# Optimization experiments

Measured on AMD Instinct MI355X. Metric: run time of the kernel, lower is better.

Reference implementation:

```python
import jax, jax.numpy as jnp
import numpy as np
from jax import lax

B, C, H, W = 4, 512, 48, 48
R = 8            # inter_rate -> spatial q/k channels = C // R
C4 = C // 4      # chl_attention query channels
N = H * W


def _conv1x1(x, w, b=None):
    # x: (B,C,H,W), w: (O,C)
    y = jnp.einsum('bchw,oc->bohw', x, w)
    if b is not None:
        y = y + b[None, :, None, None]
    return y


def _conv3x3(x, w):
    # w: (O,I,3,3), SAME padding, no bias
    return lax.conv_general_dilated(x, w, (1, 1), 'SAME',
                                    dimension_numbers=('NCHW', 'OIHW', 'NCHW'))


def _bn_relu(x, scale, bias):
    # eval-mode BatchNorm folded into per-channel scale/bias, then ReLU
    return jax.nn.relu(x * scale[None, :, None, None] + bias[None, :, None, None])


def _masked_softmax(e, mask):
    # softmax restricted to mask>0 positions (== exp(e)*mask / sum(exp(e)*mask))
    neg = jnp.finfo(e.dtype).min
    z = jnp.where(mask[None] > 0, e, neg)
    return jax.nn.softmax(z, axis=-1)


def _chl(x, qw, qs, qb, ew, eb):
    # channel attention block (chl_attention)
    b, c, h, w = x.shape
    n = h * w
    q = jnp.einsum('bchw,oc->bohw', x, qw)                 # (B,C4,H,W)
    q = jax.nn.relu(q * qs[None, :, None, None] + qb[None, :, None, None])
    q = q.reshape(b, C4, n)
    k = x.reshape(b, c, n)
    energy = jnp.einsum('bqn,bcn->bqc', q, k)              # (B,C4,C)
    expand = jnp.einsum('oq,bqc->boc', ew, energy) + eb[None, :, None]  # (B,C,C)
    en = jnp.max(expand, -1, keepdims=True) - expand
    attn = jax.nn.softmax(en, -1)                          # (B,C,C)
    out = jnp.einsum('bcd,bdn->bcn', attn, k)
    return out.reshape(b, c, h, w)


def setup_inputs() -> dict:
    key = jax.random.key(0)
    ks = jax.random.split(key, 32)
    f = jnp.float32
    s = lambda k, shp, sc: (sc * jax.random.normal(k, shp)).astype(f)
    inp = {}
    inp['x'] = s(ks[0], (B, C, H, W), 1.0)
    Cr = C // R
    inp['wq'] = s(ks[1], (Cr, C), 1.0 / np.sqrt(C))
    inp['bq'] = s(ks[2], (Cr,), 0.02)
    inp['wk'] = s(ks[3], (Cr, C), 1.0 / np.sqrt(C))
    inp['bk'] = s(ks[4], (Cr,), 0.02)
    inp['wv0'] = s(ks[5], (C, C), 1.0 / np.sqrt(C))
    inp['bv0'] = s(ks[6], (C,), 0.02)
    inp['conv1_w'] = s(ks[7], (C, C, 3, 3), 1.0 / np.sqrt(9 * C))
    inp['conv1_s'] = (1.0 + 0.1 * jax.random.normal(ks[8], (C,))).astype(f)
    inp['conv1_b'] = s(ks[9], (C,), 0.05)
    inp['conv2_w'] = s(ks[10], (C, C, 3, 3), 1.0 / np.sqrt(9 * C))
    inp['conv2_s'] = (1.0 + 0.1 * jax.random.normal(ks[11], (C,))).astype(f)
    inp['conv2_b'] = s(ks[12], (C,), 0.05)
    inp['gamma'] = jnp.full((1,), 0.5, f)
    inp['gamma1'] = jnp.full((1,), 0.5, f)
    inp['gamma2'] = jnp.full((1,), 0.5, f)
    # chl_attention #1 params
    inp['c1_qw'] = s(ks[13], (C4, C), 1.0 / np.sqrt(C))
    inp['c1_qs'] = (1.0 + 0.1 * jax.random.normal(ks[14], (C4,))).astype(f)
    inp['c1_qb'] = s(ks[15], (C4,), 0.05)
    inp['c1_ew'] = s(ks[16], (C, C4), 1.0 / np.sqrt(C4))
    inp['c1_eb'] = s(ks[17], (C,), 0.02)
    # chl_attention #2 params
    inp['c2_qw'] = s(ks[18], (C4, C), 1.0 / np.sqrt(C))
    inp['c2_qs'] = (1.0 + 0.1 * jax.random.normal(ks[19], (C4,))).astype(f)
    inp['c2_qb'] = s(ks[20], (C4,), 0.05)
    inp['c2_ew'] = s(ks[21], (C, C4), 1.0 / np.sqrt(C4))
    inp['c2_eb'] = s(ks[22], (C,), 0.02)
    # binary (N,N) masks: random sparsity + diagonal so every row has support
    eye = jnp.eye(N, dtype=f)
    m1 = (jax.random.uniform(ks[23], (N, N)) < 0.25).astype(f)
    m2 = (jax.random.uniform(ks[24], (N, N)) < 0.10).astype(f)
    inp['mask1'] = jnp.maximum(m1, eye)
    inp['mask2'] = jnp.maximum(m2, eye)
    return inp


def reference(x, wq, bq, wk, bk, wv0, bv0, conv1_w, conv1_s, conv1_b,
              conv2_w, conv2_s, conv2_b, gamma, gamma1, gamma2,
              c1_qw, c1_qs, c1_qb, c1_ew, c1_eb,
              c2_qw, c2_qs, c2_qb, c2_ew, c2_eb, mask1, mask2):
    b, c, h, w = x.shape
    n = h * w
    q = _conv1x1(x, wq, bq).reshape(b, -1, n)   # (B,Cr,N)
    k = _conv1x1(x, wk, bk).reshape(b, -1, n)   # (B,Cr,N)
    energy = jnp.einsum('bqn,bqm->bnm', q, k)   # (B,N,N)
    attn0 = jax.nn.softmax(energy, -1)
    attn1 = _masked_softmax(energy, mask1)
    attn2 = _masked_softmax(energy, mask2)
    v = _conv1x1(x, wv0, bv0).reshape(b, c, n)
    # pass 0 (unmasked)
    out0 = jnp.einsum('bcn,bmn->bcm', v, attn0).reshape(b, c, h, w)
    out0 = gamma[0] * out0 + x
    out0 = _bn_relu(_conv3x3(out0, conv1_w), conv1_s, conv1_b)
    # pass 1 (mask1, channel-attn value)
    v1 = _chl(out0, c1_qw, c1_qs, c1_qb, c1_ew, c1_eb).reshape(b, c, n)
    out1 = jnp.einsum('bcn,bmn->bcm', v1, attn1).reshape(b, c, h, w)
    out1 = gamma1[0] * out1 + out0
    out1 = _bn_relu(_conv3x3(out1, conv2_w), conv2_s, conv2_b)
    # pass 2 (mask2)
    v2 = _chl(out1, c2_qw, c2_qs, c2_qb, c2_ew, c2_eb).reshape(b, c, n)
    out2 = jnp.einsum('bcn,bmn->bcm', v2, attn2).reshape(b, c, h, w)
    out = gamma2[0] * out2 + out1
    return out
```

## Files before the change

kernel.cpp:

```cpp
#include <hip/hip_runtime.h>

#define B_  4
#define C_  512
#define H_  48
#define W_  48
#define N_  2304
#define CR_ 64
#define C4_ 128
#define TK  16
#define LDSP 68
#define PW  50
#define PN  2500
#define KW  4608

typedef short  s16x8 __attribute__((ext_vector_type(8)));
typedef float  f32x4 __attribute__((ext_vector_type(4)));

__device__ __forceinline__ unsigned short f2bf(float f) {
  union { float f; unsigned int u; } v; v.f = f;
  const unsigned int u = v.u;
  return (unsigned short)((u + 0x7FFFu + ((u >> 16) & 1u)) >> 16);
}
__device__ __forceinline__ float bf2f(unsigned short h) {
  union { unsigned int u; float f; } v; v.u = ((unsigned int)h) << 16;
// ... 356 lines not shown
      acc[1][0] = __builtin_amdgcn_mfma_f32_16x16x32_bf16(ah1, bl0, acc[1][0], 0, 0, 0);
      acc[1][1] = __builtin_amdgcn_mfma_f32_16x16x32_bf16(ah1, bl1, acc[1][1], 0, 0, 0);
      acc[0][0] = __builtin_amdgcn_mfma_f32_16x16x32_bf16(al0, bh0, acc[0][0], 0, 0, 0);
      acc[0][1] = __builtin_amdgcn_mfma_f32_16x16x32_bf16(al0, bh1, acc[0][1], 0, 0, 0);
      acc[1][0] = __builtin_amdgcn_mfma_f32_16x16x32_bf16(al1, bh0, acc[1][0], 0, 0, 0);
      acc[1][1] = __builtin_amdgcn_mfma_f32_16x16x32_bf16(al1, bh1, acc[1][1], 0, 0, 0);
    }
    __syncthreads();
  }

  float* Yb = Y + (size_t)b * ySB;
#pragma unroll
  for (int mt = 0; mt < 2; ++mt)
#pragma unroll
    for (int nt = 0; nt < 2; ++nt) {
      const int col = n0 + wn * 32 + nt * 16 + lrow;
      const int rbase = m0 + wm * 32 + mt * 16 + (lane >> 4) * 4;
#pragma unroll
      for (int i = 0; i < 4; ++i) {
        const int row = rbase + i;
        float v = acc[mt][nt][i];
        const float s  = scale ? scale[row] : 1.f;
        const float bb = bias ? bias[row] : 0.f;
        v = v * s + bb;
        if (relu) v = fmaxf(v, 0.f);
        if (outMode == 0)      Yb[(size_t)row * ldy + col] = v;
        else if (outMode == 1) Yb[(size_t)col * ldy + row] = v;
        else                   atomicAdd(Yb + (size_t)col * ldy + row, v);
      }
    }
}

__global__ __launch_bounds__(256)
void pad_split(const float* __restrict__ X, unsigned short* __restrict__ Xh,
               unsigned short* __restrict__ Xl)
{
  __shared__ float t[64][65];
  const int b = blockIdx.x, n0 = blockIdx.y * 64;
  const int tid = threadIdx.x;
  const float* Xb = X + (size_t)b * C_ * N_;
  unsigned short* Xhb = Xh + (size_t)b * PN * C_;
  unsigned short* Xlb = Xl + (size_t)b * PN * C_;
  for (int cs = 0; cs < 8; ++cs) {
    const int c0 = cs * 64;
    __syncthreads();
#pragma unroll
    for (int i = 0; i < 16; ++i) {
      const int cc = i * 4 + (tid >> 6);
      t[cc][tid & 63] = Xb[(size_t)(c0 + cc) * N_ + n0 + (tid & 63)];
    }
    __syncthreads();
    const int cc = tid & 63;
#pragma unroll
    for (int i = 0; i < 16; ++i) {
      const int nn = i * 4 + (tid >> 6);
      const int n = n0 + nn;
      const float v = t[cc][nn];
      const unsigned short hh = f2bf(v);
      const unsigned short ll = f2bf(v - bf2f(hh));
      const size_t p = (size_t)((n / 48 + 1) * PW + (n % 48) + 1) * C_ + c0 + cc;
      Xhb[p] = hh; Xlb[p] = ll;
    }
  }
}

__global__ __launch_bounds__(256)
void zero_ring(unsigned short* __restrict__ Xh, unsigned short* __restrict__ Xl)
{
  const int b = blockIdx.y, r = blockIdx.x;
  int pcol;
  if (r < 50)       pcol = r;
  else if (r < 100) pcol = 49 * PW + (r - 50);
  else if (r < 148) pcol = (r - 100 + 1) * PW;
  else              pcol = (r - 148 + 1) * PW + 49;
  unsigned int* h = (unsigned int*)(Xh + ((size_t)b * PN + pcol) * C_);
  unsigned int* l = (unsigned int*)(Xl + ((size_t)b * PN + pcol) * C_);
  h[threadIdx.x] = 0u;
  l[threadIdx.x] = 0u;
}

__global__ __launch_bounds__(256)
void wsplit(const float* __restrict__ W, unsigned short* __restrict__ Wh,
            unsigned short* __restrict__ Wl)
{
  const int o = blockIdx.x, tap = blockIdx.y;
#pragma unroll
  for (int i = 0; i < 2; ++i) {
    const int c = threadIdx.x + i * 256;
    const float v = W[(size_t)o * KW + c * 9 + tap];
    const unsigned short hh = f2bf(v);
    Wh[(size_t)o * KW + tap * C_ + c] = hh;
    Wl[(size_t)o * KW + tap * C_ + c] = f2bf(v - bf2f(hh));
  }
}

__global__ __launch_bounds__(256)
void tr_split(const float* __restrict__ X, unsigned short* __restrict__ Th,
              unsigned short* __restrict__ Tl)
{
  __shared__ float t[64][65];
  const int b = blockIdx.x, n0 = blockIdx.y * 64;
  const int tid = threadIdx.x;
  const float* Xb = X + (size_t)b * C_ * N_;
  unsigned short* Thb = Th + (size_t)b * N_ * C_;
  unsigned short* Tlb = Tl + (size_t)b * N_ * C_;
  for (int cs = 0; cs < 8; ++cs) {
    const int c0 = cs * 64;
    __syncthreads();
#pragma unroll
    for (int i = 0; i < 16; ++i) {
      const int cc = i * 4 + (tid >> 6);
      t[cc][tid & 63] = Xb[(size_t)(c0 + cc) * N_ + n0 + (tid & 63)];
    }
    __syncthreads();
    const int cc = tid & 63;
#pragma unroll
    for (int i = 0; i < 16; ++i) {
      const int nn = i * 4 + (tid >> 6);
      const float v = t[cc][nn];
      const unsigned short hh = f2bf(v);
      Thb[(size_t)(n0 + nn) * C_ + c0 + cc] = hh;
      Tlb[(size_t)(n0 + nn) * C_ + c0 + cc] = f2bf(v - bf2f(hh));
    }
  }
}

__global__ __launch_bounds__(256)
void mfma_conv2(const unsigned short* __restrict__ Xh, const unsigned short* __restrict__ Xl,
                const unsigned short* __restrict__ Wh, const unsigned short* __restrict__ Wl,
                const float* __restrict__ sc, const float* __restrict__ bi,
                float* __restrict__ Y)
{
  __shared__ unsigned short Ah[64][72], Al[64][72];
  __shared__ unsigned short Bh[64][72], Bl[64][72];
  const int b  = blockIdx.z;
  const int m0 = blockIdx.y * 64, n0 = blockIdx.x * 64;
  const int tid  = threadIdx.x;
  const int lane = tid & 63, wave = tid >> 6;
  const int wm = wave >> 1, wn = wave & 1;
  const int lrow = lane & 15, lk8 = (lane >> 4) * 8;
  const int sRow = tid >> 2, sK = (tid & 3) * 16;
  const int nj = n0 + sRow;
  const int pbase = (nj / 48 + 1) * PW + (nj % 48) + 1;
  const unsigned short* Xhb = Xh + (size_t)b * PN * C_;
  const unsigned short* Xlb = Xl + (size_t)b * PN * C_;
  f32x4 acc[2][2] = {};
  s16x8 r0, r1, r2, r3, r4, r5, r6, r7;

#define CONV_LD(IT)                                                        \
  {                                                                        \
    const int tap_ = (IT) >> 3, c0_ = ((IT) & 7) * 64;                     \
    const int t3_ = tap_ / 3;                                              \
    const int toff_ = (t3_ - 1) * PW + (tap_ - t3_ * 3 - 1);               \
    const size_t bofs_ = (size_t)(pbase + toff_) * C_ + c0_ + sK;          \
    const size_t wrow_ = (size_t)(m0 + sRow) * KW + (size_t)tap_ * C_ + c0_ + sK; \
    r0 = *(const s16x8*)(Wh + wrow_);     r1 = *(const s16x8*)(Wh + wrow_ + 8); \
    r2 = *(const s16x8*)(Wl + wrow_);     r3 = *(const s16x8*)(Wl + wrow_ + 8); \
    r4 = *(const s16x8*)(Xhb + bofs_);    r5 = *(const s16x8*)(Xhb + bofs_ + 8); \
    r6 = *(const s16x8*)(Xlb + bofs_);    r7 = *(const s16x8*)(Xlb + bofs_ + 8); \
  }

  CONV_LD(0);
  for (int it = 0; it < 72; ++it) {
    *(s16x8*)&Ah[sRow][sK] = r0; *(s16x8*)&Ah[sRow][sK + 8] = r1;
    *(s16x8*)&Al[sRow][sK] = r2; *(s16x8*)&Al[sRow][sK + 8] = r3;
    *(s16x8*)&Bh[sRow][sK] = r4; *(s16x8*)&Bh[sRow][sK + 8] = r5;
    *(s16x8*)&Bl[sRow][sK] = r6; *(s16x8*)&Bl[sRow][sK + 8] = r7;
    __syncthreads();
    if (it < 71) CONV_LD(it + 1);
#pragma unroll
    for (int kc = 0; kc < 2; ++kc) {
      const s16x8 ah0 = *(const s16x8*)&Ah[wm * 32 + lrow     ][kc * 32 + lk8];
      const s16x8 ah1 = *(const s16x8*)&Ah[wm * 32 + 16 + lrow][kc * 32 + lk8];
      const s16x8 al0 = *(const s16x8*)&Al[wm * 32 + lrow     ][kc * 32 + lk8];
      const s16x8 al1 = *(const s16x8*)&Al[wm * 32 + 16 + lrow][kc * 32 + lk8];
      const s16x8 bh0 = *(const s16x8*)&Bh[wn * 32 + lrow     ][kc * 32 + lk8];
      const s16x8 bh1 = *(const s16x8*)&Bh[wn * 32 + 16 + lrow][kc * 32 + lk8];
      const s16x8 bl0 = *(const s16x8*)&Bl[wn * 32 + lrow     ][kc * 32 + lk8];
      const s16x8 bl1 = *(const s16x8*)&Bl[wn * 32 + 16 + lrow][kc * 32 + lk8];
      acc[0][0] = __builtin_amdgcn_mfma_f32_16x16x32_bf16(ah0, bh0, acc[0][0], 0, 0, 0);
      acc[0][1] = __builtin_amdgcn_mfma_f32_16x16x32_bf16(ah0, bh1, acc[0][1], 0, 0, 0);
      acc[1][0] = __builtin_amdgcn_mfma_f32_16x16x32_bf16(ah1, bh0, acc[1][0], 0, 0, 0);
      acc[1][1] = __builtin_amdgcn_mfma_f32_16x16x32_bf16(ah1, bh1, acc[1][1], 0, 0, 0);
      acc[0][0] = __builtin_amdgcn_mfma_f32_16x16x32_bf16(ah0, bl0, acc[0][0], 0, 0, 0);
      acc[0][1] = __builtin_amdgcn_mfma_f32_16x16x32_bf16(ah0, bl1, acc[0][1], 0, 0, 0);
      acc[1][0] = __builtin_amdgcn_mfma_f32_16x16x32_bf16(ah1, bl0, acc[1][0], 0, 0, 0);
      acc[1][1] = __builtin_amdgcn_mfma_f32_16x16x32_bf16(ah1, bl1, acc[1][1], 0, 0, 0);
      acc[0][0] = __builtin_amdgcn_mfma_f32_16x16x32_bf16(al0, bh0, acc[0][0], 0, 0, 0);
      acc[0][1] = __builtin_amdgcn_mfma_f32_16x16x32_bf16(al0, bh1, acc[0][1], 0, 0, 0);
      acc[1][0] = __builtin_amdgcn_mfma_f32_16x16x32_bf16(al1, bh0, acc[1][0], 0, 0, 0);
      acc[1][1] = __builtin_amdgcn_mfma_f32_16x16x32_bf16(al1, bh1, acc[1][1], 0, 0, 0);
    }
    __syncthreads();
  }
#undef CONV_LD

  float* Yb = Y + (size_t)b * C_ * N_;
#pragma unroll
  for (int mt = 0; mt < 2; ++mt)
#pragma unroll
    for (int nt = 0; nt < 2; ++nt) {
      const int col = n0 + wn * 32 + nt * 16 + lrow;
      const int rbase = m0 + wm * 32 + mt * 16 + (lane >> 4) * 4;
#pragma unroll
      for (int i = 0; i < 4; ++i) {
        const int row = rbase + i;
        const float v = fmaxf(acc[mt][nt][i] * sc[row] + bi[row], 0.f);
        Yb[(size_t)row * N_ + col] = v;
      }
    }
}

__global__ __launch_bounds__(256)
void mfma_conv_split(const float* __restrict__ X, const float* __restrict__ Wt,
                     const float* __restrict__ sc, const float* __restrict__ bi,
                     float* __restrict__ Y)
{
  __shared__ unsigned short Ah[64][72], Al[64][72];
  __shared__ unsigned short Bh[64][72], Bl[64][72];
  const int b  = blockIdx.z;
  const int m0 = blockIdx.y * 64, n0 = blockIdx.x * 64;
  const int tid  = threadIdx.x;
  const int lane = tid & 63, wave = tid >> 6;
  const int wm = wave >> 1, wn = wave & 1;
  const int lrow = lane & 15, lk8 = (lane >> 4) * 8;
  const int sRow = tid >> 2, sK = (tid & 3) * 16;
  const int tj = tid & 63, tkg = (tid >> 6) * 16;
  const int n = n0 + tj, yy = n / W_, xx = n - yy * W_;
  const float* Xb = X + (size_t)b * C_ * N_;
  f32x4 acc[2][2] = {};

  for (int k0 = 0; k0 < KW; k0 += 64) {
    {
      const float* src = Wt + (size_t)(m0 + sRow) * KW + k0 + sK;
      unsigned short h[16], l[16];
#pragma unroll
      for (int t = 0; t < 16; ++t) {
        const float v = src[t];
        const unsigned short hh = f2bf(v);
        h[t] = hh;
        l[t] = f2bf(v - bf2f(hh));
      }
      *(s16x8*)&Ah[sRow][sK]     = *(s16x8*)&h[0];
      *(s16x8*)&Ah[sRow][sK + 8] = *(s16x8*)&h[8];
      *(s16x8*)&Al[sRow][sK]     = *(s16x8*)&l[0];
      *(s16x8*)&Al[sRow][sK + 8] = *(s16x8*)&l[8];
    }
    {
#pragma unroll
      for (int ii = 0; ii < 16; ii += 2) {
        unsigned int ph = 0, pl = 0;
#pragma unroll
        for (int hft = 0; hft < 2; ++hft) {
          const int kg = k0 + tkg + ii + hft;
          const int c = kg / 9, tap = kg - c * 9;
          const int t3 = tap / 3;
          const int iy = yy + t3 - 1, ix = xx + (tap - t3 * 3) - 1;
          float v = 0.f;
          if (iy >= 0 && iy < H_ && ix >= 0 && ix < W_)
            v = Xb[(size_t)c * N_ + iy * W_ + ix];
          const unsigned short hh = f2bf(v);
          const unsigned short ll = f2bf(v - bf2f(hh));
          ph |= ((unsigned int)hh) << (16 * hft);
          pl |= ((unsigned int)ll) << (16 * hft);
        }
        *(unsigned int*)&Bh[tj][tkg + ii] = ph;
        *(unsigned int*)&Bl[tj][tkg + ii] = pl;
      }
    }
    __syncthreads();
#pragma unroll
    for (int kc = 0; kc < 2; ++kc) {
      const s16x8 ah0 = *(const s16x8*)&Ah[wm * 32 + lrow     ][kc * 32 + lk8];
      const s16x8 ah1 = *(const s16x8*)&Ah[wm * 32 + 16 + lrow][kc * 32 + lk8];
      const s16x8 al0 = *(const s16x8*)&Al[wm * 32 + lrow     ][kc * 32 + lk8];
      const s16x8 al1 = *(const s16x8*)&Al[wm * 32 + 16 + lrow][kc * 32 + lk8];
      const s16x8 bh0 = *(const s16x8*)&Bh[wn * 32 + lrow     ][kc * 32 + lk8];
      const s16x8 bh1 = *(const s16x8*)&Bh[wn * 32 + 16 + lrow][kc * 32 + lk8];
      const s16x8 bl0 = *(const s16x8*)&Bl[wn * 32 + lrow     ][kc * 32 + lk8];
      const s16x8 bl1 = *(const s16x8*)&Bl[wn * 32 + 16 + lrow][kc * 32 + lk8];
      acc[0][0] = __builtin_amdgcn_mfma_f32_16x16x32_bf16(ah0, bh0, acc[0][0], 0, 0, 0);
      acc[0][1] = __builtin_amdgcn_mfma_f32_16x16x32_bf16(ah0, bh1, acc[0][1], 0, 0, 0);
      acc[1][0] = __builtin_amdgcn_mfma_f32_16x16x32_bf16(ah1, bh0, acc[1][0], 0, 0, 0);
      acc[1][1] = __builtin_amdgcn_mfma_f32_16x16x32_bf16(ah1, bh1, acc[1][1], 0, 0, 0);
      acc[0][0] = __builtin_amdgcn_mfma_f32_16x16x32_bf16(ah0, bl0, acc[0][0], 0, 0, 0);
      acc[0][1] = __builtin_amdgcn_mfma_f32_16x16x32_bf16(ah0, bl1, acc[0][1], 0, 0, 0);
      acc[1][0] = __builtin_amdgcn_mfma_f32_16x16x32_bf16(ah1, bl0, acc[1][0], 0, 0, 0);
      acc[1][1] = __builtin_amdgcn_mfma_f32_16x16x32_bf16(ah1, bl1, acc[1][1], 0, 0, 0);
      acc[0][0] = __builtin_amdgcn_mfma_f32_16x16x32_bf16(al0, bh0, acc[0][0], 0, 0, 0);
      acc[0][1] = __builtin_amdgcn_mfma_f32_16x16x32_bf16(al0, bh1, acc[0][1], 0, 0, 0);
      acc[1][0] = __builtin_amdgcn_mfma_f32_16x16x32_bf16(al1, bh0, acc[1][0], 0, 0, 0);
      acc[1][1] = __builtin_amdgcn_mfma_f32_16x16x32_bf16(al1, bh1, acc[1][1], 0, 0, 0);
    }
    __syncthreads();
  }

  float* Yb = Y + (size_t)b * C_ * N_;
#pragma unroll
  for (int mt = 0; mt < 2; ++mt)
#pragma unroll
    for (int nt = 0; nt < 2; ++nt) {
      const int col = n0 + wn * 32 + nt * 16 + lrow;
      const int rbase = m0 + wm * 32 + mt * 16 + (lane >> 4) * 4;
#pragma unroll
      for (int i = 0; i < 4; ++i) {
        const int row = rbase + i;
        const float v = fmaxf(acc[mt][nt][i] * sc[row] + bi[row], 0.f);
        Yb[(size_t)row * N_ + col] = v;
      }
    }
}

__global__ __launch_bounds__(256)
void build_P(const float* __restrict__ E, const float* __restrict__ st,
             int variant, const float* __restrict__ mask,
             unsigned short* __restrict__ P)
{
  const int m = blockIdx.x, b = blockIdx.y, t = threadIdx.x;
  const float* sp = st + ((size_t)b * N_ + m) * 6 + variant * 2;
  const float mx = sp[0], rs = 1.f / sp[1];
  const float* Er = E + ((size_t)b * N_ + m) * N_;
  unsigned short* Pr = P + ((size_t)b * N_ + m) * N_;
  const float* Mr = mask ? mask + (size_t)m * N_ : nullptr;
#pragma unroll
  for (int i = 0; i < 9; ++i) {
    const int idx = t + i * 256;
    float w = __expf(Er[idx] - mx) * rs;
    if (Mr && !(Mr[idx] > 0.f)) w = 0.f;
    Pr[idx] = f2bf(w);
  }
}

__global__ __launch_bounds__(256)
void softmax_stats(const float* __restrict__ E, const float* __restrict__ M1,
                   const float* __restrict__ M2, float* __restrict__ st)
{
  const int row = blockIdx.x, b = blockIdx.y, tid = threadIdx.x;
  const float* er = E + ((size_t)b * N_ + row) * N_;
  const float* r1 = M1 + (size_t)row * N_;
  const float* r2 = M2 + (size_t)row * N_;
  float mx0 = -3.4e38f, mx1 = -3.4e38f, mx2 = -3.4e38f;
  for (int n = tid; n < N_; n += 256) {
    const float v = er[n];
    mx0 = fmaxf(mx0, v);
    if (r1[n] > 0.f) mx1 = fmaxf(mx1, v);
    if (r2[n] > 0.f) mx2 = fmaxf(mx2, v);
  }
  __shared__ float red[256];
  mx0 = blockReduceMax(mx0, red);
  mx1 = blockReduceMax(mx1, red);
  mx2 = blockReduceMax(mx2, red);
  float s0 = 0.f, s1 = 0.f, s2 = 0.f;
  for (int n = tid; n < N_; n += 256) {
    const float v = er[n];
    s0 += __expf(v - mx0);
    if (r1[n] > 0.f) s1 += __expf(v - mx1);
    if (r2[n] > 0.f) s2 += __expf(v - mx2);
  }
  s0 = blockReduceSum(s0, red);
  s1 = blockReduceSum(s1, red);
  s2 = blockReduceSum(s2, red);
  if (tid == 0) {
    float* o = st + ((size_t)b * N_ + row) * 6;
// ... 226 lines not shown
  const float* c2w    = (const float*)d_in[10];
  const float* c2s    = (const float*)d_in[11];
  const float* c2b    = (const float*)d_in[12];
  const float* gamma  = (const float*)d_in[13];
  const float* gamma1 = (const float*)d_in[14];
  const float* gamma2 = (const float*)d_in[15];
  const float* c1qw   = (const float*)d_in[16];
  const float* c1qs   = (const float*)d_in[17];
  const float* c1qb   = (const float*)d_in[18];
  const float* c1ew   = (const float*)d_in[19];
  const float* c1eb   = (const float*)d_in[20];
  const float* c2qw   = (const float*)d_in[21];
  const float* c2qs   = (const float*)d_in[22];
  const float* c2qb   = (const float*)d_in[23];
  const float* c2ew   = (const float*)d_in[24];
  const float* c2eb   = (const float*)d_in[25];
  const float* mask1  = (const float*)d_in[26];
  const float* mask2  = (const float*)d_in[27];

  const size_t QK = 589824;
  const size_t CQ = 1179648;
  const size_t VV = 4718592;
  const size_t EE = 21233664;
  const size_t ST = 55296;
  const size_t CE = 262144;
  const size_t CA = 1048576;
  const size_t ELEMS_B = CQ + VV + EE + ST + VV + CE + CA;
  const size_t ELEMS_A = ELEMS_B + EE / 2;
  const int tier = (ws_size >= ELEMS_A * 4) ? 0
                 : (ws_size >= ELEMS_B * 4) ? 1 : 2;

  float* ws = (float*)d_ws;
  float *qbuf, *kbuf, *cq, *vbuf, *ebuf, *stb, *o0, *ce1, *cat_;
  unsigned short *Pbuf = nullptr, *Xh = nullptr, *Xl = nullptr,
                 *Whs = nullptr, *Wls = nullptr,
                 *xTh = nullptr, *xTl = nullptr, *oTh = nullptr, *oTl = nullptr;
  float *qTf = nullptr, *kTf = nullptr;
  if (tier <= 1) {
    qbuf = ws; kbuf = ws + QK;
    cq   = ws;
    vbuf = ws + CQ;
    ebuf = vbuf + VV;
    stb  = ebuf + EE;
    o0   = stb + ST;
    ce1  = o0 + VV;
    cat_ = ce1 + CE;
    if (tier == 0) {
      unsigned short* reg = (unsigned short*)(cat_ + CA);
      xTh = reg;
      xTl = reg + 4718592;
      qTf = (float*)(reg + 9437184);
      kTf = qTf + 589824;
      Pbuf = reg;
      Xh  = reg;
      Xl  = reg + 5120000;
      Whs = reg + 10240000;
      Wls = reg + 12599296;
      oTh = reg;
      oTl = reg + 4718592;
    }
  } else {
    qbuf = ws; kbuf = qbuf + QK;
    cq   = kbuf + QK;
    vbuf = cq + CQ;
    stb  = vbuf + VV;
    o0   = stb + ST;
    ce1  = o0 + VV;
    cat_ = ce1 + CE;
    ebuf = nullptr;
  }
  float* t0 = (float*)d_out;
  unsigned short* vb16 = (unsigned short*)vbuf;

  const dim3 TPB(256);
  const long long sxc = (long long)C_ * N_;
  const long long sqr = (long long)CR_ * N_;
  const long long sq4 = (long long)C4_ * N_;
  const long long sNN = (long long)N_ * N_;
  const long long sNC = (long long)N_ * C_;
  const long long sCC = (long long)C_ * C_;
  const long long sEC = (long long)C4_ * C_;
  const long long sNR = (long long)N_ * CR_;

  if (tier == 0) {
    tr_split<<<dim3(B_, 36), TPB, 0, stream>>>(x, xTh, xTl);
    mfma_sp<<<dim3(36, 1, 4), TPB, 0, stream>>>(wq, 0, C_, xTh, xTl, sNC, C_, 1,
        qTf, sNR, CR_, 1, C_, 1, nullptr, bq, 0);
    mfma_sp<<<dim3(36, 1, 4), TPB, 0, stream>>>(wk, 0, C_, xTh, xTl, sNC, C_, 1,
        kTf, sNR, CR_, 1, C_, 1, nullptr, bk, 0);
    mfma_gemm<<<dim3(36, 8, 4), TPB, 0, stream>>>(wv0, 0, 0, C_, xTh, sNC, C_, 2,
        vb16, 1, sxc, N_, C_, nullptr, bv0, 0, nullptr, nullptr, 0);
    mfma_sp<<<dim3(36, 36, 4), TPB, 0, stream>>>(qTf, sNR, CR_, kTf, nullptr, sNR, CR_, 0,
        ebuf, sNN, N_, 0, CR_, 1, nullptr, nullptr, 0);
    softmax_stats<<<dim3(N_, 4), TPB, 0, stream>>>(ebuf, mask1, mask2, stb);
  } else if (tier == 1) {
    gemm_nn<<<dim3(36, 1, 4), TPB, 0, stream>>>(wq, 0, C_, x, sxc, N_,
                                                qbuf, sqr, N_, C_, nullptr, bq, 0);
    gemm_nn<<<dim3(36, 1, 4), TPB, 0, stream>>>(wk, 0, C_, x, sxc, N_,
                                                kbuf, sqr, N_, C_, nullptr, bk, 0);
    mfma_gemm<<<dim3(36, 8, 4), TPB, 0, stream>>>(wv0, 0, 0, C_, x, sxc, N_, 1,
        vbuf, 0, sxc, N_, C_, nullptr, bv0, 0, nullptr, nullptr, 0);
    gemm_tn<<<dim3(36, 36, 4), TPB, 0, stream>>>(qbuf, sqr, N_, kbuf, sqr, N_,
                                                 ebuf, sNN, N_, CR_);
    softmax_stats<<<dim3(N_, 4), TPB, 0, stream>>>(ebuf, mask1, mask2, stb);
  } else {
    gemm_nn<<<dim3(36, 1, 4), TPB, 0, stream>>>(wq, 0, C_, x, sxc, N_,
                                                qbuf, sqr, N_, C_, nullptr, bq, 0);
    gemm_nn<<<dim3(36, 1, 4), TPB, 0, stream>>>(wk, 0, C_, x, sxc, N_,
                                                kbuf, sqr, N_, C_, nullptr, bk, 0);
    mfma_gemm<<<dim3(36, 8, 4), TPB, 0, stream>>>(wv0, 0, 0, C_, x, sxc, N_, 1,
        vbuf, 0, sxc, N_, C_, nullptr, bv0, 0, nullptr, nullptr, 0);
    softmax_stats_rq<<<dim3(N_, 4), TPB, 0, stream>>>(qbuf, kbuf, mask1, mask2, stb);
  }

  for (int pass = 0; pass < 3; ++pass) {
    const float* msk = (pass == 0) ? nullptr : (pass == 1 ? mask1 : mask2);
    const float* gm  = (pass == 0) ? gamma : (pass == 1 ? gamma1 : gamma2);
    const float* res = (pass == 0) ? x : o0;
    float* dst = (pass == 2) ? (float*)d_out : t0;

    if (tier == 0) {
      build_P<<<dim3(N_, 4), TPB, 0, stream>>>(ebuf, stb, pass, msk, Pbuf);
      mfma_gemm<<<dim3(36, 8, 4), TPB, 0, stream>>>(vb16, 1, sxc, N_, Pbuf, sNN, N_, 2,
          dst, 0, sxc, N_, N_, nullptr, nullptr, 0, gm, res, sxc);
    } else if (tier == 1) {
      attn_apply<<<dim3(36, 8, 4), TPB, 0, stream>>>(vbuf, ebuf, stb, pass, msk,
                                                     gm, res, dst);
    } else {
      attn_apply_rq<<<dim3(36, 8, 4), TPB, 0, stream>>>(vbuf, qbuf, kbuf, stb, pass, msk,
                                                        gm, res, dst);
    }
    if (pass == 2) break;

    const float* cw = (pass == 0) ? c1w : c2w;
    const float* cs = (pass == 0) ? c1s : c2s;
    const float* cb = (pass == 0) ? c1b : c2b;
    if (tier == 0) {
      pad_split<<<dim3(B_, 36), TPB, 0, stream>>>(dst, Xh, Xl);
      zero_ring<<<dim3(196, B_), TPB, 0, stream>>>(Xh, Xl);
      wsplit<<<dim3(512, 9), TPB, 0, stream>>>(cw, Whs, Wls);
      mfma_conv2<<<dim3(36, 8, 4), TPB, 0, stream>>>(Xh, Xl, Whs, Wls, cs, cb, o0);
    } else {
      mfma_conv_split<<<dim3(36, 8, 4), TPB, 0, stream>>>(dst, cw, cs, cb, o0);
    }

    const float* qw = (pass == 0) ? c1qw : c2qw;
    const float* qs = (pass == 0) ? c1qs : c2qs;
    const float* qb = (pass == 0) ? c1qb : c2qb;
    const float* ew = (pass == 0) ? c1ew : c2ew;
    const float* eb = (pass == 0) ? c1eb : c2eb;
    if (tier == 0) {
      tr_split<<<dim3(B_, 36), TPB, 0, stream>>>(o0, oTh, oTl);
      mfma_sp<<<dim3(36, 2, 4), TPB, 0, stream>>>(qw, 0, C_, oTh, oTl, sNC, C_, 1,
          cq, sq4, N_, 0, C_, 1, qs, qb, 1);
      zero_buf<<<dim3(256), TPB, 0, stream>>>((float4*)ce1, (int)(CE / 4));
      mfma_sp<<<dim3(8, 2, 16), TPB, 0, stream>>>(cq, sq4, N_, o0, nullptr, sxc, N_, 0,
          ce1, sEC, C4_, 2, N_, 4, nullptr, nullptr, 0);
      mfma_sp<<<dim3(8, 8, 4), TPB, 0, stream>>>(ew, 0, C4_, ce1, nullptr, sEC, C4_, 0,
          cat_, sCC, C_, 0, C4_, 1, nullptr, eb, 0);
      chl_softmax<<<dim3(C_ * 4), TPB, 0, stream>>>(cat_);
      mfma_gemm<<<dim3(36, 8, 4), TPB, 0, stream>>>(cat_, 0, sCC, C_, oTh, sNC, C_, 2,
          vb16, 1, sxc, N_, C_, nullptr, nullptr, 0, nullptr, nullptr, 0);
    } else {
      gemm_nn<<<dim3(36, 2, 4), TPB, 0, stream>>>(qw, 0, C_, o0, sxc, N_,
                                                  cq, sq4, N_, C_, qs, qb, 1);
      zero_buf<<<dim3(256), TPB, 0, stream>>>((float4*)ce1, (int)(CE / 4));
      gemm_nt_splitk<<<dim3(8, 2, 16), TPB, 0, stream>>>(cq, sq4, N_, o0, sxc, N_,
                                                         ce1, sEC, C_, N_);
      gemm_nn<<<dim3(8, 8, 4), TPB, 0, stream>>>(ew, 0, C4_, ce1, sEC, C_,
                                                 cat_, sCC, C_, C4_, nullptr, eb, 0);
      chl_softmax<<<dim3(C_ * 4), TPB, 0, stream>>>(cat_);
      mfma_gemm<<<dim3(36, 8, 4), TPB, 0, stream>>>(cat_, 0, sCC, C_, o0, sxc, N_, 1,
          vbuf, 0, sxc, N_, C_, nullptr, nullptr, 0, nullptr, nullptr, 0);
    }
  }
// ... 2 lines not shown
```

Baseline: 1.305 ms.

## Fuse softmax weights into attention-apply GEMM, widen conv tiles, hoist weight splits

```diff
diff --git a/kernel.cpp b/kernel.cpp
--- a/kernel.cpp
+++ b/kernel.cpp
@@ -412,15 +412,29 @@
 }
 
 __global__ __launch_bounds__(256)
-void pad_split(const float* __restrict__ X, unsigned short* __restrict__ Xh,
-               unsigned short* __restrict__ Xl)
-{
-  __shared__ float t[64][65];
-  const int b = blockIdx.x, n0 = blockIdx.y * 64;
+void pad_split2(const float* __restrict__ X, unsigned short* __restrict__ Xh,
+                unsigned short* __restrict__ Xl)
+{
+  const int b = blockIdx.x;
   const int tid = threadIdx.x;
-  const float* Xb = X + (size_t)b * C_ * N_;
   unsigned short* Xhb = Xh + (size_t)b * PN * C_;
   unsigned short* Xlb = Xl + (size_t)b * PN * C_;
+  if (blockIdx.y == 36) {
+    for (int idx = tid; idx < 196 * 256; idx += 256) {
+      const int r = idx >> 8, u = idx & 255;
+      int pcol;
+      if (r < 50)       pcol = r;
+      else if (r < 100) pcol = 49 * PW + (r - 50);
+      else if (r < 148) pcol = (r - 100 + 1) * PW;
+      else              pcol = (r - 148 + 1) * PW + 49;
+      ((unsigned int*)(Xhb + (size_t)pcol * C_))[u] = 0u;
+      ((unsigned int*)(Xlb + (size_t)pcol * C_))[u] = 0u;
+    }
+    return;
+  }
+  __shared__ float t[64][65];
+  const int n0 = blockIdx.y * 64;
+  const float* Xb = X + (size_t)b * C_ * N_;
   for (int cs = 0; cs < 8; ++cs) {
     const int c0 = cs * 64;
     __syncthreads();
@@ -445,21 +459,6 @@
 }
 
 __global__ __launch_bounds__(256)
-void zero_ring(unsigned short* __restrict__ Xh, unsigned short* __restrict__ Xl)
-{
-  const int b = blockIdx.y, r = blockIdx.x;
-  int pcol;
-  if (r < 50)       pcol = r;
-  else if (r < 100) pcol = 49 * PW + (r - 50);
-  else if (r < 148) pcol = (r - 100 + 1) * PW;
-  else              pcol = (r - 148 + 1) * PW + 49;
-  unsigned int* h = (unsigned int*)(Xh + ((size_t)b * PN + pcol) * C_);
-  unsigned int* l = (unsigned int*)(Xl + ((size_t)b * PN + pcol) * C_);
-  h[threadIdx.x] = 0u;
-  l[threadIdx.x] = 0u;
-}
-
-__global__ __launch_bounds__(256)
 void wsplit(const float* __restrict__ W, unsigned short* __restrict__ Wh,
             unsigned short* __restrict__ Wl)
 {
@@ -506,10 +505,209 @@
 }
 
 __global__ __launch_bounds__(256)
-void mfma_conv2(const unsigned short* __restrict__ Xh, const unsigned short* __restrict__ Xl,
+void mfma_conv3(const unsigned short* __restrict__ Xh, const unsigned short* __restrict__ Xl,
                 const unsigned short* __restrict__ Wh, const unsigned short* __restrict__ Wl,
                 const float* __restrict__ sc, const float* __restrict__ bi,
                 float* __restrict__ Y)
+{
+  __shared__ unsigned short Ah[128][72], Al[128][72];
+  __shared__ unsigned short Bh[64][72], Bl[64][72];
+  const int b  = blockIdx.z;
+  const int m0 = blockIdx.y * 128, n0 = blockIdx.x * 64;
+  const int tid  = threadIdx.x;
+  const int lane = tid & 63, wave = tid >> 6;
+  const int wm = wave >> 1, wn = wave & 1;
+  const int lrow = lane & 15, lk8 = (lane >> 4) * 8;
+  const int aRow = tid >> 1, aK = (tid & 1) * 32;
+  const int bRow = tid >> 2, bK = (tid & 3) * 16;
+  const int nj = n0 + bRow;
+  const int pbase = (nj / 48 + 1) * PW + (nj % 48) + 1;
+  const unsigned short* Xhb = Xh + (size_t)b * PN * C_;
+  const unsigned short* Xlb = Xl + (size_t)b * PN * C_;
+  f32x4 acc[4][2] = {};
+  s16x8 a0h, a1h, a2h, a3h, a0l, a1l, a2l, a3l, b0h, b1h, b0l, b1l;
+
+#define CONV_LD(IT)                                                             \
+  {                                                                             \
+    const int tap_ = (IT) >> 3, c0_ = ((IT) & 7) * 64;                          \
+    const int t3_ = tap_ / 3;                                                   \
+    const int toff_ = (t3_ - 1) * PW + (tap_ - t3_ * 3 - 1);                    \
+    const size_t bofs_ = (size_t)(pbase + toff_) * C_ + c0_ + bK;               \
+    const size_t wrow_ = (size_t)(m0 + aRow) * KW + (size_t)tap_ * C_ + c0_ + aK; \
+    a0h = *(const s16x8*)(Wh + wrow_);      a1h = *(const s16x8*)(Wh + wrow_ + 8);  \
+    a2h = *(const s16x8*)(Wh + wrow_ + 16); a3h = *(const s16x8*)(Wh + wrow_ + 24); \
+    a0l = *(const s16x8*)(Wl + wrow_);      a1l = *(const s16x8*)(Wl + wrow_ + 8);  \
+    a2l = *(const s16x8*)(Wl + wrow_ + 16); a3l = *(const s16x8*)(Wl + wrow_ + 24); \
+    b0h = *(const s16x8*)(Xhb + bofs_);     b1h = *(const s16x8*)(Xhb + bofs_ + 8); \
+    b0l = *(const s16x8*)(Xlb + bofs_);     b1l = *(const s16x8*)(Xlb + bofs_ + 8); \
+  }
+
+  CONV_LD(0);
+  for (int it = 0; it < 72; ++it) {
+    *(s16x8*)&Ah[aRow][aK]      = a0h; *(s16x8*)&Ah[aRow][aK + 8]  = a1h;
+    *(s16x8*)&Ah[aRow][aK + 16] = a2h; *(s16x8*)&Ah[aRow][aK + 24] = a3h;
+    *(s16x8*)&Al[aRow][aK]      = a0l; *(s16x8*)&Al[aRow][aK + 8]  = a1l;
+    *(s16x8*)&Al[aRow][aK + 16] = a2l; *(s16x8*)&Al[aRow][aK + 24] = a3l;
+    *(s16x8*)&Bh[bRow][bK]      = b0h; *(s16x8*)&Bh[bRow][bK + 8]  = b1h;
+    *(s16x8*)&Bl[bRow][bK]      = b0l; *(s16x8*)&Bl[bRow][bK + 8]  = b1l;
+    __syncthreads();
+    if (it < 71) CONV_LD(it + 1);
+#pragma unroll
+    for (int kc = 0; kc < 2; ++kc) {
+      s16x8 ah[4], al[4], bh[2], bl[2];
+#pragma unroll
+      for (int mt = 0; mt < 4; ++mt) {
+        ah[mt] = *(const s16x8*)&Ah[wm * 64 + mt * 16 + lrow][kc * 32 + lk8];
+        al[mt] = *(const s16x8*)&Al[wm * 64 + mt * 16 + lrow][kc * 32 + lk8];
+      }
+#pragma unroll
+      for (int nt = 0; nt < 2; ++nt) {
+        bh[nt] = *(const s16x8*)&Bh[wn * 32 + nt * 16 + lrow][kc * 32 + lk8];
+        bl[nt] = *(const s16x8*)&Bl[wn * 32 + nt * 16 + lrow][kc * 32 + lk8];
+      }
+#pragma unroll
+      for (int mt = 0; mt < 4; ++mt)
+#pragma unroll
+        for (int nt = 0; nt < 2; ++nt) {
+          acc[mt][nt] = __builtin_amdgcn_mfma_f32_16x16x32_bf16(ah[mt], bh[nt], acc[mt][nt], 0, 0, 0);
+          acc[mt][nt] = __builtin_amdgcn_mfma_f32_16x16x32_bf16(ah[mt], bl[nt], acc[mt][nt], 0, 0, 0);
+          acc[mt][nt] = __builtin_amdgcn_mfma_f32_16x16x32_bf16(al[mt], bh[nt], acc[mt][nt], 0, 0, 0);
+        }
+    }
+    __syncthreads();
+  }
+#undef CONV_LD
+
+  float* Yb = Y + (size_t)b * C_ * N_;
+#pragma unroll
+  for (int mt = 0; mt < 4; ++mt)
+#pragma unroll
+    for (int nt = 0; nt < 2; ++nt) {
+      const int col = n0 + wn * 32 + nt * 16 + lrow;
+      const int rbase = m0 + wm * 64 + mt * 16 + (lane >> 4) * 4;
+#pragma unroll
+      for (int i = 0; i < 4; ++i) {
+        const int row = rbase + i;
+        const float v = fmaxf(acc[mt][nt][i] * sc[row] + bi[row], 0.f);
+        Yb[(size_t)row * N_ + col] = v;
+      }
+    }
+}
+
+__global__ __launch_bounds__(256)
+void mfma_apply(const unsigned short* __restrict__ V, const float* __restrict__ E,
+                const float* __restrict__ st, int variant,
+                const float* __restrict__ mask,
+                const float* __restrict__ gammaPtr,
+                const float* __restrict__ Resid, float* __restrict__ Y)
+{
+  __shared__ unsigned short As[128][72];
+  __shared__ unsigned short Bs[64][72];
+  const int b  = blockIdx.z;
+  const int c0 = blockIdx.y * 128, m0 = blockIdx.x * 64;
+  const int tid  = threadIdx.x;
+  const int lane = tid & 63, wave = tid >> 6;
+  const int wm = wave >> 1, wn = wave & 1;
+  const int lrow = lane & 15, lk8 = (lane >> 4) * 8;
+  const int aRow = tid >> 1, aK = (tid & 1) * 32;
+  const int bRow = tid >> 2, bK = (tid & 3) * 16;
+  const int mrow = m0 + bRow;
+  const float* sp = st + ((size_t)b * N_ + mrow) * 6 + variant * 2;
+  const float mx = sp[0], rs = 1.f / sp[1];
+  const unsigned short* Vb = V + (size_t)b * C_ * N_;
+  const float* Er = E + ((size_t)b * N_ + mrow) * N_;
+  const float* Mr = mask ? mask + (size_t)mrow * N_ : nullptr;
+  f32x4 acc[4][2] = {};
+  s16x8 a0, a1, a2, a3;
+  float4 e0, e1, e2, e3, q0, q1, q2, q3;
+
+#define APPLY_LD(K0)                                                      \
+  {                                                                       \
+    const unsigned short* s = Vb + (size_t)(c0 + aRow) * N_ + (K0) + aK;  \
+    a0 = *(const s16x8*)(s);      a1 = *(const s16x8*)(s + 8);            \
+    a2 = *(const s16x8*)(s + 16); a3 = *(const s16x8*)(s + 24);           \
+    const float* e = Er + (K0) + bK;                                      \
+    e0 = *(const float4*)(e);     e1 = *(const float4*)(e + 4);           \
+    e2 = *(const float4*)(e + 8); e3 = *(const float4*)(e + 12);          \
+    if (Mr) {                                                             \
+      const float* m = Mr + (K0) + bK;                                    \
+      q0 = *(const float4*)(m);     q1 = *(const float4*)(m + 4);         \
+      q2 = *(const float4*)(m + 8); q3 = *(const float4*)(m + 12);        \
+    }                                                                     \
+  }
+
+  APPLY_LD(0);
+  for (int k0 = 0; k0 < N_; k0 += 64) {
+    *(s16x8*)&As[aRow][aK]      = a0; *(s16x8*)&As[aRow][aK + 8]  = a1;
+    *(s16x8*)&As[aRow][aK + 16] = a2; *(s16x8*)&As[aRow][aK + 24] = a3;
+    {
+      float w[16];
+      const float4 ee[4] = {e0, e1, e2, e3};
+      const float4 qq[4] = {q0, q1, q2, q3};
+#pragma unroll
+      for (int g4 = 0; g4 < 4; ++g4) {
+        const float4 e4 = ee[g4];
+        w[g4 * 4 + 0] = __expf(e4.x - mx) * rs;
+        w[g4 * 4 + 1] = __expf(e4.y - mx) * rs;
+        w[g4 * 4 + 2] = __expf(e4.z - mx) * rs;
+        w[g4 * 4 + 3] = __expf(e4.w - mx) * rs;
+        if (Mr) {
+          const float4 m4 = qq[g4];
+          if (!(m4.x > 0.f)) w[g4 * 4 + 0] = 0.f;
+          if (!(m4.y > 0.f)) w[g4 * 4 + 1] = 0.f;
+          if (!(m4.z > 0.f)) w[g4 * 4 + 2] = 0.f;
+          if (!(m4.w > 0.f)) w[g4 * 4 + 3] = 0.f;
+        }
+      }
+      s16x8 p0, p1;
+#pragma unroll
+      for (int t = 0; t < 8; ++t) { p0[t] = (short)f2bf(w[t]); p1[t] = (short)f2bf(w[8 + t]); }
+      *(s16x8*)&Bs[bRow][bK]     = p0;
+      *(s16x8*)&Bs[bRow][bK + 8] = p1;
+    }
+    __syncthreads();
+    if (k0 + 64 < N_) APPLY_LD(k0 + 64);
+#pragma unroll
+    for (int kc = 0; kc < 2; ++kc) {
+      s16x8 av[4], bv[2];
+#pragma unroll
+      for (int mt = 0; mt < 4; ++mt)
+        av[mt] = *(const s16x8*)&As[wm * 64 + mt * 16 + lrow][kc * 32 + lk8];
+#pragma unroll
+      for (int nt = 0; nt < 2; ++nt)
+        bv[nt] = *(const s16x8*)&Bs[wn * 32 + nt * 16 + lrow][kc * 32 + lk8];
+#pragma unroll
+      for (int mt = 0; mt < 4; ++mt)
+#pragma unroll
+        for (int nt = 0; nt < 2; ++nt)
+          acc[mt][nt] = __builtin_amdgcn_mfma_f32_16x16x32_bf16(av[mt], bv[nt], acc[mt][nt], 0, 0, 0);
+    }
+    __syncthreads();
+  }
+#undef APPLY_LD
+
+  const float g = gammaPtr[0];
+  float* Yb = Y + (size_t)b * C_ * N_;
+  const float* Rb = Resid + (size_t)b * C_ * N_;
+#pragma unroll
+  for (int mt = 0; mt < 4; ++mt)
+#pragma unroll
+    for (int nt = 0; nt < 2; ++nt) {
+      const int col = m0 + wn * 32 + nt * 16 + lrow;
+      const int rbase = c0 + wm * 64 + mt * 16 + (lane >> 4) * 4;
+#pragma unroll
+      for (int i = 0; i < 4; ++i) {
+        const int row = rbase + i;
+        const size_t off = (size_t)row * N_ + col;
+        Yb[off] = g * acc[mt][nt][i] + Rb[off];
+      }
+    }
+}
+
+__global__ __launch_bounds__(256)
+void mfma_conv_split(const float* __restrict__ X, const float* __restrict__ Wt,
+                     const float* __restrict__ sc, const float* __restrict__ bi,
+                     float* __restrict__ Y)
 {
   __shared__ unsigned short Ah[64][72], Al[64][72];
   __shared__ unsigned short Bh[64][72], Bl[64][72];
@@ -520,34 +718,50 @@
   const int wm = wave >> 1, wn = wave & 1;
   const int lrow = lane & 15, lk8 = (lane >> 4) * 8;
   const int sRow = tid >> 2, sK = (tid & 3) * 16;
-  const int nj = n0 + sRow;
-  const int pbase = (nj / 48 + 1) * PW + (nj % 48) + 1;
-  const unsigned short* Xhb = Xh + (size_t)b * PN * C_;
-  const unsigned short* Xlb = Xl + (size_t)b * PN * C_;
+  const int tj = tid & 63, tkg = (tid >> 6) * 16;
+  const int n = n0 + tj, yy = n / W_, xx = n - yy * W_;
+  const float* Xb = X + (size_t)b * C_ * N_;
   f32x4 acc[2][2] = {};
-  s16x8 r0, r1, r2, r3, r4, r5, r6, r7;
-
-#define CONV_LD(IT)                                                        \
-  {                                                                        \
-    const int tap_ = (IT) >> 3, c0_ = ((IT) & 7) * 64;                     \
-    const int t3_ = tap_ / 3;                                              \
-    const int toff_ = (t3_ - 1) * PW + (tap_ - t3_ * 3 - 1);               \
-    const size_t bofs_ = (size_t)(pbase + toff_) * C_ + c0_ + sK;          \
-    const size_t wrow_ = (size_t)(m0 + sRow) * KW + (size_t)tap_ * C_ + c0_ + sK; \
-    r0 = *(const s16x8*)(Wh + wrow_);     r1 = *(const s16x8*)(Wh + wrow_ + 8); \
-    r2 = *(const s16x8*)(Wl + wrow_);     r3 = *(const s16x8*)(Wl + wrow_ + 8); \
-    r4 = *(const s16x8*)(Xhb + bofs_);    r5 = *(const s16x8*)(Xhb + bofs_ + 8); \
-    r6 = *(const s16x8*)(Xlb + bofs_);    r7 = *(const s16x8*)(Xlb + bofs_ + 8); \
-  }
-
-  CONV_LD(0);
-  for (int it = 0; it < 72; ++it) {
-    *(s16x8*)&Ah[sRow][sK] = r0; *(s16x8*)&Ah[sRow][sK + 8] = r1;
-    *(s16x8*)&Al[sRow][sK] = r2; *(s16x8*)&Al[sRow][sK + 8] = r3;
-    *(s16x8*)&Bh[sRow][sK] = r4; *(s16x8*)&Bh[sRow][sK + 8] = r5;
-    *(s16x8*)&Bl[sRow][sK] = r6; *(s16x8*)&Bl[sRow][sK + 8] = r7;
-    __syncthreads();
-    if (it < 71) CONV_LD(it + 1);
+
+  for (int k0 = 0; k0 < KW; k0 += 64) {
+    {
+      const float* src = Wt + (size_t)(m0 + sRow) * KW + k0 + sK;
+      unsigned short h[16], l[16];
+#pragma unroll
+      for (int t = 0; t < 16; ++t) {
+        const float v = src[t];
+        const unsigned short hh = f2bf(v);
+        h[t] = hh;
+        l[t] = f2bf(v - bf2f(hh));
+      }
+      *(s16x8*)&Ah[sRow][sK]     = *(s16x8*)&h[0];
+      *(s16x8*)&Ah[sRow][sK + 8] = *(s16x8*)&h[8];
+      *(s16x8*)&Al[sRow][sK]     = *(s16x8*)&l[0];
+      *(s16x8*)&Al[sRow][sK + 8] = *(s16x8*)&l[8];
+    }
+    {
+#pragma unroll
+      for (int ii = 0; ii < 16; ii += 2) {
+        unsigned int ph = 0, pl = 0;
+#pragma unroll
+        for (int hft = 0; hft < 2; ++hft) {
+          const int kg = k0 + tkg + ii + hft;
+          const int c = kg / 9, tap = kg - c * 9;
+          const int t3 = tap / 3;
+          const int iy = yy + t3 - 1, ix = xx + (tap - t3 * 3) - 1;
+          float v = 0.f;
+          if (iy >= 0 && iy < H_ && ix >= 0 && ix < W_)
+            v = Xb[(size_t)c * N_ + iy * W_ + ix];
+          const unsigned short hh = f2bf(v);
+          const unsigned short ll = f2bf(v - bf2f(hh));
+          ph |= ((unsigned int)hh) << (16 * hft);
+          pl |= ((unsigned int)ll) << (16 * hft);
+        }
+        *(unsigned int*)&Bh[tj][tkg + ii] = ph;
+        *(unsigned int*)&Bl[tj][tkg + ii] = pl;
+      }
+    }
+    __syncthreads();
 #pragma unroll
     for (int kc = 0; kc < 2; ++kc) {
       const s16x8 ah0 = *(const s16x8*)&Ah[wm * 32 + lrow     ][kc * 32 + lk8];
@@ -573,7 +787,6 @@
     }
     __syncthreads();
   }
-#undef CONV_LD
 
   float* Yb = Y + (size_t)b * C_ * N_;
 #pragma unroll
@@ -589,126 +802,6 @@
         Yb[(size_t)row * N_ + col] = v;
       }
     }
-}
-
-__global__ __launch_bounds__(256)
-void mfma_conv_split(const float* __restrict__ X, const float* __restrict__ Wt,
-                     const float* __restrict__ sc, const float* __restrict__ bi,
-                     float* __restrict__ Y)
-{
-  __shared__ unsigned short Ah[64][72], Al[64][72];
-  __shared__ unsigned short Bh[64][72], Bl[64][72];
-  const int b  = blockIdx.z;
-  const int m0 = blockIdx.y * 64, n0 = blockIdx.x * 64;
-  const int tid  = threadIdx.x;
-  const int lane = tid & 63, wave = tid >> 6;
-  const int wm = wave >> 1, wn = wave & 1;
-  const int lrow = lane & 15, lk8 = (lane >> 4) * 8;
-  const int sRow = tid >> 2, sK = (tid & 3) * 16;
-  const int tj = tid & 63, tkg = (tid >> 6) * 16;
-  const int n = n0 + tj, yy = n / W_, xx = n - yy * W_;
-  const float* Xb = X + (size_t)b * C_ * N_;
-  f32x4 acc[2][2] = {};
-
-  for (int k0 = 0; k0 < KW; k0 += 64) {
-    {
-      const float* src = Wt + (size_t)(m0 + sRow) * KW + k0 + sK;
-      unsigned short h[16], l[16];
-#pragma unroll
-      for (int t = 0; t < 16; ++t) {
-        const float v = src[t];
-        const unsigned short hh = f2bf(v);
-        h[t] = hh;
-        l[t] = f2bf(v - bf2f(hh));
-      }
-      *(s16x8*)&Ah[sRow][sK]     = *(s16x8*)&h[0];
-      *(s16x8*)&Ah[sRow][sK + 8] = *(s16x8*)&h[8];
-      *(s16x8*)&Al[sRow][sK]     = *(s16x8*)&l[0];
-      *(s16x8*)&Al[sRow][sK + 8] = *(s16x8*)&l[8];
-    }
-    {
-#pragma unroll
-      for (int ii = 0; ii < 16; ii += 2) {
-        unsigned int ph = 0, pl = 0;
-#pragma unroll
-        for (int hft = 0; hft < 2; ++hft) {
-          const int kg = k0 + tkg + ii + hft;
-          const int c = kg / 9, tap = kg - c * 9;
-          const int t3 = tap / 3;
-          const int iy = yy + t3 - 1, ix = xx + (tap - t3 * 3) - 1;
-          float v = 0.f;
-          if (iy >= 0 && iy < H_ && ix >= 0 && ix < W_)
-            v = Xb[(size_t)c * N_ + iy * W_ + ix];
-          const unsigned short hh = f2bf(v);
-          const unsigned short ll = f2bf(v - bf2f(hh));
-          ph |= ((unsigned int)hh) << (16 * hft);
-          pl |= ((unsigned int)ll) << (16 * hft);
-        }
-        *(unsigned int*)&Bh[tj][tkg + ii] = ph;
-        *(unsigned int*)&Bl[tj][tkg + ii] = pl;
-      }
-    }
-    __syncthreads();
-#pragma unroll
-    for (int kc = 0; kc < 2; ++kc) {
-      const s16x8 ah0 = *(const s16x8*)&Ah[wm * 32 + lrow     ][kc * 32 + lk8];
-      const s16x8 ah1 = *(const s16x8*)&Ah[wm * 32 + 16 + lrow][kc * 32 + lk8];
-      const s16x8 al0 = *(const s16x8*)&Al[wm * 32 + lrow     ][kc * 32 + lk8];
-      const s16x8 al1 = *(const s16x8*)&Al[wm * 32 + 16 + lrow][kc * 32 + lk8];
-      const s16x8 bh0 = *(const s16x8*)&Bh[wn * 32 + lrow     ][kc * 32 + lk8];
-      const s16x8 bh1 = *(const s16x8*)&Bh[wn * 32 + 16 + lrow][kc * 32 + lk8];
-      const s16x8 bl0 = *(const s16x8*)&Bl[wn * 32 + lrow     ][kc * 32 + lk8];
-      const s16x8 bl1 = *(const s16x8*)&Bl[wn * 32 + 16 + lrow][kc * 32 + lk8];
-      acc[0][0] = __builtin_amdgcn_mfma_f32_16x16x32_bf16(ah0, bh0, acc[0][0], 0, 0, 0);
-      acc[0][1] = __builtin_amdgcn_mfma_f32_16x16x32_bf16(ah0, bh1, acc[0][1], 0, 0, 0);
-      acc[1][0] = __builtin_amdgcn_mfma_f32_16x16x32_bf16(ah1, bh0, acc[1][0], 0, 0, 0);
-      acc[1][1] = __builtin_amdgcn_mfma_f32_16x16x32_bf16(ah1, bh1, acc[1][1], 0, 0, 0);
-      acc[0][0] = __builtin_amdgcn_mfma_f32_16x16x32_bf16(ah0, bl0, acc[0][0], 0, 0, 0);
-      acc[0][1] = __builtin_amdgcn_mfma_f32_16x16x32_bf16(ah0, bl1, acc[0][1], 0, 0, 0);
-      acc[1][0] = __builtin_amdgcn_mfma_f32_16x16x32_bf16(ah1, bl0, acc[1][0], 0, 0, 0);
-      acc[1][1] = __builtin_amdgcn_mfma_f32_16x16x32_bf16(ah1, bl1, acc[1][1], 0, 0, 0);
-      acc[0][0] = __builtin_amdgcn_mfma_f32_16x16x32_bf16(al0, bh0, acc[0][0], 0, 0, 0);
-      acc[0][1] = __builtin_amdgcn_mfma_f32_16x16x32_bf16(al0, bh1, acc[0][1], 0, 0, 0);
-      acc[1][0] = __builtin_amdgcn_mfma_f32_16x16x32_bf16(al1, bh0, acc[1][0], 0, 0, 0);
-      acc[1][1] = __builtin_amdgcn_mfma_f32_16x16x32_bf16(al1, bh1, acc[1][1], 0, 0, 0);
-    }
-    __syncthreads();
-  }
-
-  float* Yb = Y + (size_t)b * C_ * N_;
-#pragma unroll
-  for (int mt = 0; mt < 2; ++mt)
-#pragma unroll
-    for (int nt = 0; nt < 2; ++nt) {
-      const int col = n0 + wn * 32 + nt * 16 + lrow;
-      const int rbase = m0 + wm * 32 + mt * 16 + (lane >> 4) * 4;
-#pragma unroll
-      for (int i = 0; i < 4; ++i) {
-        const int row = rbase + i;
-        const float v = fmaxf(acc[mt][nt][i] * sc[row] + bi[row], 0.f);
-        Yb[(size_t)row * N_ + col] = v;
-      }
-    }
-}
-
-__global__ __launch_bounds__(256)
-void build_P(const float* __restrict__ E, const float* __restrict__ st,
-             int variant, const float* __restrict__ mask,
-             unsigned short* __restrict__ P)
-{
-  const int m = blockIdx.x, b = blockIdx.y, t = threadIdx.x;
-  const float* sp = st + ((size_t)b * N_ + m) * 6 + variant * 2;
-  const float mx = sp[0], rs = 1.f / sp[1];
-  const float* Er = E + ((size_t)b * N_ + m) * N_;
-  unsigned short* Pr = P + ((size_t)b * N_ + m) * N_;
-  const float* Mr = mask ? mask + (size_t)m * N_ : nullptr;
-#pragma unroll
-  for (int i = 0; i < 9; ++i) {
-    const int idx = t + i * 256;
-    float w = __expf(Er[idx] - mx) * rs;
-    if (Mr && !(Mr[idx] > 0.f)) w = 0.f;
-    Pr[idx] = f2bf(w);
-  }
 }
 
 __global__ __launch_bounds__(256)
@@ -1001,8 +1094,8 @@
 
   float* ws = (float*)d_ws;
   float *qbuf, *kbuf, *cq, *vbuf, *ebuf, *stb, *o0, *ce1, *cat_;
-  unsigned short *Pbuf = nullptr, *Xh = nullptr, *Xl = nullptr,
-                 *Whs = nullptr, *Wls = nullptr,
+  unsigned short *Xh = nullptr, *Xl = nullptr,
+                 *W1h = nullptr, *W1l = nullptr, *W2h = nullptr, *W2l = nullptr,
                  *xTh = nullptr, *xTl = nullptr, *oTh = nullptr, *oTl = nullptr;
   float *qTf = nullptr, *kTf = nullptr;
   if (tier <= 1) {
@@ -1020,11 +1113,12 @@
       xTl = reg + 4718592;
       qTf = (float*)(reg + 9437184);
       kTf = qTf + 589824;
-      Pbuf = reg;
+      W1h = reg + 11796480;
+      W1l = reg + 14155776;
+      W2h = reg + 16515072;
+      W2l = reg + 18874368;
       Xh  = reg;
       Xl  = reg + 5120000;
-      Whs = reg + 10240000;
-      Wls = reg + 12599296;
       oTh = reg;
       oTl = reg + 4718592;
     }
@@ -1062,6 +1156,8 @@
     mfma_sp<<<dim3(36, 36, 4), TPB, 0, stream>>>(qTf, sNR, CR_, kTf, nullptr, sNR, CR_, 0,
         ebuf, sNN, N_, 0, CR_, 1, nullptr, nullptr, 0);
     softmax_stats<<<dim3(N_, 4), TPB, 0, stream>>>(ebuf, mask1, mask2, stb);
+    wsplit<<<dim3(512, 9), TPB, 0, stream>>>(c1w, W1h, W1l);
+    wsplit<<<dim3(512, 9), TPB, 0, stream>>>(c2w, W2h, W2l);
   } else if (tier == 1) {
     gemm_nn<<<dim3(36, 1, 4), TPB, 0, stream>>>(wq, 0, C_, x, sxc, N_,
                                                 qbuf, sqr, N_, C_, nullptr, bq, 0);
@@ -1089,9 +1185,8 @@
     float* dst = (pass == 2) ? (float*)d_out : t0;
 
     if (tier == 0) {
-      build_P<<<dim3(N_, 4), TPB, 0, stream>>>(ebuf, stb, pass, msk, Pbuf);
-      mfma_gemm<<<dim3(36, 8, 4), TPB, 0, stream>>>(vb16, 1, sxc, N_, Pbuf, sNN, N_, 2,
-          dst, 0, sxc, N_, N_, nullptr, nullptr, 0, gm, res, sxc);
+      mfma_apply<<<dim3(36, 4, 4), TPB, 0, stream>>>(vb16, ebuf, stb, pass, msk,
+                                                     gm, res, dst);
     } else if (tier == 1) {
       attn_apply<<<dim3(36, 8, 4), TPB, 0, stream>>>(vbuf, ebuf, stb, pass, msk,
                                                      gm, res, dst);
@@ -1101,15 +1196,14 @@
     }
     if (pass == 2) break;
 
-    const float* cw = (pass == 0) ? c1w : c2w;
     const float* cs = (pass == 0) ? c1s : c2s;
     const float* cb = (pass == 0) ? c1b : c2b;
     if (tier == 0) {
-      pad_split<<<dim3(B_, 36), TPB, 0, stream>>>(dst, Xh, Xl);
-      zero_ring<<<dim3(196, B_), TPB, 0, stream>>>(Xh, Xl);
-      wsplit<<<dim3(512, 9), TPB, 0, stream>>>(cw, Whs, Wls);
-      mfma_conv2<<<dim3(36, 8, 4), TPB, 0, stream>>>(Xh, Xl, Whs, Wls, cs, cb, o0);
+      pad_split2<<<dim3(B_, 37), TPB, 0, stream>>>(dst, Xh, Xl);
+      mfma_conv3<<<dim3(36, 4, 4), TPB, 0, stream>>>(Xh, Xl,
+          (pass == 0) ? W1h : W2h, (pass == 0) ? W1l : W2l, cs, cb, o0);
     } else {
+      const float* cw = (pass == 0) ? c1w : c2w;
       mfma_conv_split<<<dim3(36, 8, 4), TPB, 0, stream>>>(dst, cw, cs, cb, o0);
     }
 
```

After: 1.283 ms. About the same (-1.6%).
